# Kernel optimization log

Measured on AMD Instinct MI355X. Metric: run time of the kernel, lower is better.

The kernel has to match this reference:

```python
import jax, jax.numpy as jnp
import numpy as np

N_CROPS = 64
K = 128          # keypoints per crop (uniform ragged special case)
D = 128          # descriptor dim
KNN = 20
NQ = 20
MIN_V, MAX_V = 0.0, 1.0


def setup_inputs() -> dict:
    key = jax.random.key(0)
    k1, k2 = jax.random.split(key)
    b = N_CROPS * K
    anc = jax.random.normal(k1, (b, D), dtype=jnp.float32)
    pos = jax.random.normal(k2, (b, D), dtype=jnp.float32)
    # L2-normalized descriptors so similarities fall in the quantizer range
    anc = anc / jnp.linalg.norm(anc, axis=1, keepdims=True)
    pos = pos / jnp.linalg.norm(pos, axis=1, keepdims=True)
    kpts_crop_ids = np.full((N_CROPS,), K, dtype=np.int32)
    return {"anc_feat": anc, "pos_feat": pos, "kpts_crop_ids": kpts_crop_ids}


def _neg_cols(n_crops, k, b):
    # Static per-crop column indices into sim_neg_all (width b-1), excluding
    # the same-crop negative block [i*k, i*k + (k-1)) exactly as the torch code.
    all_c = np.arange(b - 1)
    cols = []
    for i in range(n_crops):
        c = i * k
        cols.append(np.concatenate([all_c[:c], all_c[c + k - 1:]]))
    return np.stack(cols)  # [n_crops, b-k]


def compute_ap(x, label, nq=NQ, min_v=MIN_V, max_v=MAX_V):
    # R2D2 APLoss.compute_AP: fixed 1x1-conv quantizer -> triangular bins
    a = (nq - 1) / (max_v - min_v)
    w1 = np.full(nq, -a, np.float32)
    b1 = (a * min_v + np.arange(nq, 0, -1)).astype(np.float32)
    w2 = np.full(nq, a, np.float32)
    b2 = (np.arange(2 - nq, 2) - a * min_v).astype(np.float32)
    w1[0], b1[0] = 0.0, 1.0     # first line of 1st half: horizontal
    w2[-1], b2[-1] = 0.0, 1.0   # last line of 2nd half: horizontal
    xq = x[:, None, :]
    q = jnp.minimum(w1[None, :, None] * xq + b1[None, :, None],
                    w2[None, :, None] * xq + b2[None, :, None])
    q = jnp.clip(q, 0.0)                                 # N x Q x M
    nbs = q.sum(-1)                                      # N x Q
    rec = (q * label[:, None, :]).sum(-1)                # N x Q
    prec = jnp.cumsum(rec, -1) / (1e-16 + jnp.cumsum(nbs, -1))
    rec = rec / rec.sum(-1, keepdims=True)
    return (prec * rec).sum(-1)                          # per-query AP, [N]


def reference(anc_feat, pos_feat, kpts_crop_ids):
    ks = np.asarray(kpts_crop_ids)
    assert np.all(ks == ks[0]) and int(ks[0]) > 1, "uniform crops, >1 kpt each"
    k = int(ks[0]); n_crops = ks.shape[0]; b = n_crops * k
    sim = anc_feat @ pos_feat.T                          # [b, b]
    sim_pos = jnp.diagonal(sim)[:, None]                 # [b, 1]
    # drop diagonal -> [b, b-1] (row-major off-diagonal, same as mtx[~eye])
    sim_neg_all = sim.reshape(-1)[:-1].reshape(b - 1, b + 1)[:, 1:].reshape(b, b - 1)
    cols = jnp.asarray(_neg_cols(n_crops, k, b))         # [n_crops, b-k]
    blocks = sim_neg_all.reshape(n_crops, k, b - 1)
    # exclude same-crop negatives per crop (static gather), then hard-neg top-k
    excl = jnp.take_along_axis(blocks, cols[:, None, :], axis=2)  # [n_crops, k, b-k]
    top, _ = jax.lax.top_k(excl, KNN)                    # sorted descending == sort[:, :knn]
    sim_neg = top.reshape(b, KNN)
    sim_final = jnp.concatenate([sim_pos, sim_neg], axis=1)      # [b, knn+1]
    lbl_final = jnp.zeros_like(sim_final).at[:, 0].set(1.0)
    ap = compute_ap(sim_final, lbl_final)
    return (1.0 - ap).mean(), ap.mean()
```

## Files before the change

kernel.cpp:

```cpp
#include <hip/hip_runtime.h>

#define B_TOT 8192
#define DIM 128
#define KNN 20
#define NQ 20

typedef float f32x4 __attribute__((ext_vector_type(4)));
typedef short short8 __attribute__((ext_vector_type(8)));

__device__ __forceinline__ unsigned short f2bf(float f) {
  unsigned u = __float_as_uint(f);
  return (unsigned short)((u + 0x7FFFu + ((u >> 16) & 1u)) >> 16);
}

__global__ __launch_bounds__(256) void cvt_bf16(
    const float* __restrict__ a, const float* __restrict__ p,
    unsigned short* __restrict__ ab, unsigned short* __restrict__ pb) {
  const int i = (blockIdx.x * 256 + threadIdx.x) * 4;
  const float4 va = *reinterpret_cast<const float4*>(a + i);
  const float4 vp = *reinterpret_cast<const float4*>(p + i);
  ushort4 ra, rp;
  ra.x = f2bf(va.x); ra.y = f2bf(va.y); ra.z = f2bf(va.z); ra.w = f2bf(va.w);
  rp.x = f2bf(vp.x); rp.y = f2bf(vp.y); rp.z = f2bf(vp.z); rp.w = f2bf(vp.w);
  *reinterpret_cast<ushort4*>(ab + i) = ra;
  *reinterpret_cast<ushort4*>(pb + i) = rp;
}

#define RPB 32
#define NTHR 512
#define NSTEP 64
#define CPS 128
#define SPAD 36

__global__ __launch_bounds__(512) void apk_mfma(
    const unsigned short* __restrict__ ancb,
    const unsigned short* __restrict__ posb,
    float* __restrict__ apsum)
{
  __shared__ __align__(16) float sSimT[CPS][SPAD];
  __shared__ float sTop[RPB][16][KNN];
  __shared__ float sDiag[RPB];
  __shared__ float sAp[RPB];

  const int tid = threadIdx.x;
  const int wave = tid >> 6;
  const int lane = tid & 63;
  const int rt = wave >> 2;
  const int cg = wave & 3;
  const int l15 = lane & 15;
  const int g = lane >> 4;
  const int rBase = blockIdx.x * RPB;
  const int cropLo = rBase & ~127;
  const int s_ex = cropLo >> 7;

  const int scanRow = tid & 31;
  const int scanChunk = tid >> 5;

  short8 afr[4];
  {
    const short8* arow = reinterpret_cast<const short8*>(
        ancb + (size_t)(rBase + rt * 16 + l15) * DIM);
    afr[0] = arow[0 + g];
    afr[1] = arow[4 + g];
    afr[2] = arow[8 + g];
    afr[3] = arow[12 + g];
  }

  float tk[KNN];
#pragma unroll
  for (int q = 0; q < KNN; ++q) tk[q] = -1e30f;

  const unsigned short* bbase = posb + (size_t)(cg * 32 + l15) * DIM + g * 8;

  short8 b0[2][4], b1[2][4];

#define LOADB(BUF, S)                                                         \
  {                                                                           \
    const unsigned short* bp = bbase + (size_t)(S) * (CPS * DIM);             \
    _Pragma("unroll") for (int n = 0; n < 2; ++n) {                           \
      _Pragma("unroll") for (int kk = 0; kk < 4; ++kk) {                      \
        (BUF)[n][kk] =                                                        \
            *reinterpret_cast<const short8*>(bp + n * (16 * DIM) + kk * 32);  \
      }                                                                       \
    }                                                                         \
  }

#define STEP_BODY(CUR, NXT, S)                                                \
  {                                                                           \
    if ((S) + 1 < NSTEP) LOADB(NXT, (S) + 1);                                 \
    f32x4 acc[2];                                                             \
    _Pragma("unroll") for (int n = 0; n < 2; ++n) {                           \
      acc[n] = 0.f;                                                           \
      _Pragma("unroll") for (int kk = 0; kk < 4; ++kk)                        \
        acc[n] = __builtin_amdgcn_mfma_f32_16x16x32_bf16(                     \
            afr[kk], (CUR)[n][kk], acc[n], 0, 0, 0);                          \
    }                                                                         \
    __syncthreads();                       \
    _Pragma("unroll") for (int n = 0; n < 2; ++n) {                           \
      const int c = cg * 32 + n * 16 + l15;                                   \
      *reinterpret_cast<f32x4*>(&sSimT[c][rt * 16 + g * 4]) = acc[n];         \
    }                                                                         \
    if ((S) == s_ex) {           \
      _Pragma("unroll") for (int n = 0; n < 2; ++n) {                         \
        if (cg * 32 + n * 16 == rBase - cropLo + rt * 16) {                   \
          _Pragma("unroll") for (int q = 0; q < 4; ++q)                       \
            if (l15 == 4 * g + q) sDiag[rt * 16 + l15] = acc[n][q];           \
        }                                                                     \
      }                                                                       \
    }                                                                         \
    __syncthreads();                                      \
    if ((S) != s_ex) {                                                        \
      _Pragma("unroll") for (int i = 0; i < 8; ++i) {                         \
        const float v = sSimT[scanChunk * 8 + i][scanRow];                    \
        if (v > tk[0]) {                                                      \
          float x = v;                                                        \
          _Pragma("unroll") for (int p = 0; p < KNN - 1; ++p) {               \
            const float nxt = tk[p + 1];                                      \
            tk[p] = fminf(x, nxt);                                            \
            x = fmaxf(x, nxt);                                                \
          }                                                                   \
          tk[KNN - 1] = x;                                                    \
        }                                                                     \
      }                                                                       \
    }                                                                         \
  }

  LOADB(b0, 0);
  for (int s = 0; s < NSTEP; s += 2) {
    STEP_BODY(b0, b1, s);
    STEP_BODY(b1, b0, s + 1);
  }

  __syncthreads();
  const int myRow = scanRow;
  const int myLane = scanChunk;
#pragma unroll
  for (int q = 0; q < KNN; ++q) sTop[myRow][myLane][q] = tk[q];
  __syncthreads();
  for (int step = 8; step > 0; step >>= 1) {
    if (myLane < step) {
      float out[KNN];
      int a = KNN - 1, b = KNN - 1;
#pragma unroll
      for (int o = KNN - 1; o >= 0; --o) {
        const float va = (a >= 0) ? sTop[myRow][myLane][a] : -3e30f;
        const float vb = (b >= 0) ? sTop[myRow][myLane + step][b] : -3e30f;
        if (va >= vb) { out[o] = va; --a; } else { out[o] = vb; --b; }
      }
#pragma unroll
      for (int q = 0; q < KNN; ++q) sTop[myRow][myLane][q] = out[q];
    }
    __syncthreads();
  }

  if (tid < RPB) {
    float x[KNN + 1];
    x[0] = sDiag[tid];
#pragma unroll
    for (int q = 0; q < KNN; ++q) x[q + 1] = sTop[tid][0][q];
    float cum_rec = 0.f, cum_nbs = 0.f, ap_num = 0.f;
#pragma unroll 1
    for (int qi = 0; qi < NQ; ++qi) {
      const float w1 = (qi == 0) ? 0.f : -19.f;
      const float c1 = (qi == 0) ? 1.f : (float)(20 - qi);
      const float w2 = (qi == NQ - 1) ? 0.f : 19.f;
      const float c2 = (qi == NQ - 1) ? 1.f : (float)(qi - 18);
      float nbs = 0.f, rec = 0.f;
#pragma unroll
      for (int jx = 0; jx < KNN + 1; ++jx) {
        const float xv = x[jx];
        float qv = fminf(fmaf(w1, xv, c1), fmaf(w2, xv, c2));
        qv = fmaxf(qv, 0.f);
        nbs += qv;
        if (jx == 0) rec = qv;
      }
      cum_rec += rec;
      cum_nbs += nbs;
      ap_num = fmaf(cum_rec / (1e-16f + cum_nbs), rec, ap_num);
    }
    sAp[tid] = ap_num / cum_rec;
  }
  __syncthreads();
  if (tid == 0) {
    float s = 0.f;
#pragma unroll
    for (int r = 0; r < RPB; ++r) s += sAp[r];
    atomicAdd(apsum, s);
  }
}

#define F_TM 16
#define F_TN 256
#define F_NTILE (B_TOT / F_TN)
#define F_TPR (F_TN / F_TM)
#define F_SSTRIDE 264
#define KCROP 128

__global__ __launch_bounds__(256) void apk_topk_f32(
    const float* __restrict__ anc, const float* __restrict__ pos,
    float* __restrict__ apsum)
{
  __shared__ __align__(16) float sAnc[F_TM][DIM];
  __shared__ float sSim[F_TM * F_SSTRIDE];
  __shared__ float sTop[F_TM][F_TPR][KNN];
  __shared__ float sDiag[F_TM];
  __shared__ float sAp[F_TM];

  const int tid = threadIdx.x;
  const int rowBase = blockIdx.x * F_TM;
  for (int idx = tid; idx < F_TM * DIM; idx += 256)
    sAnc[idx / DIM][idx % DIM] = anc[rowBase * DIM + idx];
  __syncthreads();

  float tk[KNN];
#pragma unroll
  for (int q = 0; q < KNN; ++q) tk[q] = -1e30f;
  const int cropLo = (rowBase >> 7) << 7;
  const int myRow = tid / F_TPR;
  const int myLane = tid % F_TPR;

  for (int t = 0; t < F_NTILE; ++t) {
    const int j = t * F_TN + tid;
    float acc[F_TM];
#pragma unroll
    for (int r = 0; r < F_TM; ++r) acc[r] = 0.f;
    const float4* pj = reinterpret_cast<const float4*>(pos + (size_t)j * DIM);
#pragma unroll 2
    for (int k4 = 0; k4 < DIM / 4; ++k4) {
      const float4 p = pj[k4];
#pragma unroll
      for (int r = 0; r < F_TM; ++r) {
        const float4 a = *reinterpret_cast<const float4*>(&sAnc[r][k4 * 4]);
        acc[r] = fmaf(p.x, a.x, acc[r]);
        acc[r] = fmaf(p.y, a.y, acc[r]);
        acc[r] = fmaf(p.z, a.z, acc[r]);
        acc[r] = fmaf(p.w, a.w, acc[r]);
      }
    }
    if (j >= rowBase && j < rowBase + F_TM) sDiag[j - rowBase] = acc[j - rowBase];
    __syncthreads();
#pragma unroll
    for (int r = 0; r < F_TM; ++r) sSim[r * F_SSTRIDE + tid] = acc[r];
    __syncthreads();
    const int jbase = t * F_TN;
#pragma unroll
    for (int q = 0; q < F_TN / F_TPR; ++q) {
      const int jj = q * F_TPR + myLane;
      const int jg = jbase + jj;
      const float v = sSim[myRow * F_SSTRIDE + jj];
      if ((unsigned)(jg - cropLo) >= (unsigned)KCROP && v > tk[0]) {
        float x = v;
#pragma unroll
        for (int p = 0; p < KNN - 1; ++p) {
          const float nxt = tk[p + 1];
          tk[p] = fminf(x, nxt);
          x = fmaxf(x, nxt);
        }
        tk[KNN - 1] = x;
      }
    }
  }
  __syncthreads();
#pragma unroll
  for (int q = 0; q < KNN; ++q) sTop[myRow][myLane][q] = tk[q];
  __syncthreads();
  for (int step = F_TPR / 2; step > 0; step >>= 1) {
    if (myLane < step) {
      float out[KNN];
      int a = KNN - 1, b = KNN - 1;
#pragma unroll
      for (int o = KNN - 1; o >= 0; --o) {
        const float va = (a >= 0) ? sTop[myRow][myLane][a] : -3e30f;
        const float vb = (b >= 0) ? sTop[myRow][myLane + step][b] : -3e30f;
        if (va >= vb) { out[o] = va; --a; } else { out[o] = vb; --b; }
      }
#pragma unroll
      for (int q = 0; q < KNN; ++q) sTop[myRow][myLane][q] = out[q];
    }
    __syncthreads();
  }
  if (tid < F_TM) {
    float x[KNN + 1];
    x[0] = sDiag[tid];
#pragma unroll
    for (int q = 0; q < KNN; ++q) x[q + 1] = sTop[tid][0][q];
    float cum_rec = 0.f, cum_nbs = 0.f, ap_num = 0.f;
#pragma unroll 1
    for (int qi = 0; qi < NQ; ++qi) {
      const float w1 = (qi == 0) ? 0.f : -19.f;
      const float c1 = (qi == 0) ? 1.f : (float)(20 - qi);
      const float w2 = (qi == NQ - 1) ? 0.f : 19.f;
      const float c2 = (qi == NQ - 1) ? 1.f : (float)(qi - 18);
      float nbs = 0.f, rec = 0.f;
#pragma unroll
      for (int jx = 0; jx < KNN + 1; ++jx) {
        const float xv = x[jx];
        float qv = fminf(fmaf(w1, xv, c1), fmaf(w2, xv, c2));
        qv = fmaxf(qv, 0.f);
        nbs += qv;
        if (jx == 0) rec = qv;
      }
      cum_rec += rec;
      cum_nbs += nbs;
      ap_num = fmaf(cum_rec / (1e-16f + cum_nbs), rec, ap_num);
    }
    sAp[tid] = ap_num / cum_rec;
  }
  __syncthreads();
  if (tid == 0) {
    float s = 0.f;
#pragma unroll
    for (int r = 0; r < F_TM; ++r) s += sAp[r];
    atomicAdd(apsum, s);
  }
}

__global__ void apk_final(const float* __restrict__ apsum, float* __restrict__ out) {
  const float m = *apsum * (1.f / (float)B_TOT);
  out[0] = 1.f - m;
  out[1] = m;
}

extern "C" void kernel_launch(void* const* d_in, const int* in_sizes, int n_in,
                              void* d_out, int out_size, void* d_ws, size_t ws_size,
                              hipStream_t stream) {
  const float* anc = (const float*)d_in[0];
  const float* pos = (const float*)d_in[1];
  const size_t bf_bytes = (size_t)B_TOT * DIM * sizeof(unsigned short);
  const size_t need = 2 * bf_bytes + 16;
  if (ws_size >= need) {
    unsigned short* ancb = (unsigned short*)d_ws;
    unsigned short* posb = ancb + (size_t)B_TOT * DIM;
    float* apsum = (float*)((char*)d_ws + 2 * bf_bytes);
    hipMemsetAsync(apsum, 0, sizeof(float), stream);
    cvt_bf16<<<(B_TOT * DIM) / (256 * 4), 256, 0, stream>>>(anc, pos, ancb, posb);
    apk_mfma<<<B_TOT / RPB, NTHR, 0, stream>>>(ancb, posb, apsum);
    apk_final<<<1, 1, 0, stream>>>(apsum, (float*)d_out);
  } else {
    float* apsum = (float*)d_ws;
    hipMemsetAsync(apsum, 0, sizeof(float), stream);
    apk_topk_f32<<<B_TOT / F_TM, 256, 0, stream>>>(anc, pos, apsum);
    apk_final<<<1, 1, 0, stream>>>(apsum, (float*)d_out);
  }
}
```

Baseline: 257.1 us.

## Split columns into slices with threshold-filtered candidate buffers and a separate reduce kernel

Replaces the per-block full-row scan with a grid of 128-row by 1024-column slices. Each wave filters MFMA results against a per-row running threshold and appends survivors to a bf16 shared buffer. The buffer is compacted to a top-20 only when it fills or at the end, and a second kernel merges the eight per-slice top lists in global memory and computes AP. This removes the per-step shared-memory transpose and the insertion sort over every similarity, in exchange for atomics, an extra kernel, and bf16-rounded candidate values that may change the result.

```diff
diff --git a/kernel.cpp b/kernel.cpp
--- a/kernel.cpp
+++ b/kernel.cpp
@@ -5,12 +5,22 @@
 #define KNN 20
 #define NQ 20
 
+#define RPB 128
+#define SLICE 1024
+#define NSLICE 8
+#define NSTEP 16
+#define CBUF 128
+#define FLAG_AT 63
+
 typedef float f32x4 __attribute__((ext_vector_type(4)));
 typedef short short8 __attribute__((ext_vector_type(8)));
 
 __device__ __forceinline__ unsigned short f2bf(float f) {
   unsigned u = __float_as_uint(f);
   return (unsigned short)((u + 0x7FFFu + ((u >> 16) & 1u)) >> 16);
+}
+__device__ __forceinline__ float bf2f(unsigned short u) {
+  return __uint_as_float(((unsigned)u) << 16);
 }
 
 __global__ __launch_bounds__(256) void cvt_bf16(
@@ -26,118 +36,308 @@
   *reinterpret_cast<ushort4*>(pb + i) = rp;
 }
 
-#define RPB 32
-#define NTHR 512
-#define NSTEP 64
-#define CPS 128
-#define SPAD 36
-
-__global__ __launch_bounds__(512) void apk_mfma(
+__global__ __launch_bounds__(512, 4) void apk_slice(
     const unsigned short* __restrict__ ancb,
     const unsigned short* __restrict__ posb,
-    float* __restrict__ apsum)
+    unsigned short* __restrict__ gTop,
+    float* __restrict__ gDiag)
 {
-  __shared__ __align__(16) float sSimT[CPS][SPAD];
-  __shared__ float sTop[RPB][16][KNN];
-  __shared__ float sDiag[RPB];
-  __shared__ float sAp[RPB];
+  __shared__ unsigned short sBuf[RPB][CBUF];
+  __shared__ float sMrg[RPB][4][KNN + 1];
+  __shared__ int sCnt[RPB];
+  __shared__ float sThr[RPB];
+  __shared__ int sFlag;
 
   const int tid = threadIdx.x;
   const int wave = tid >> 6;
   const int lane = tid & 63;
-  const int rt = wave >> 2;
-  const int cg = wave & 3;
+  const int rt = wave >> 1;
+  const int cg = wave & 1;
   const int l15 = lane & 15;
   const int g = lane >> 4;
-  const int rBase = blockIdx.x * RPB;
-  const int cropLo = rBase & ~127;
-  const int s_ex = cropLo >> 7;
-
-  const int scanRow = tid & 31;
-  const int scanChunk = tid >> 5;
-
-  short8 afr[4];
-  {
+  const int rg = blockIdx.x >> 3;
+  const int cs = blockIdx.x & 7;
+  const int rBase = rg * RPB;
+  const int sx0 = (cs == (rg >> 3)) ? (rg & 7) * 2 : -9;
+
+  for (int i = tid; i < RPB; i += 512) { sCnt[i] = 0; sThr[i] = -1e30f; }
+  if (tid == 0) sFlag = 0;
+  __syncthreads();
+
+  short8 afr[2][4];
+#pragma unroll
+  for (int rsub = 0; rsub < 2; ++rsub) {
     const short8* arow = reinterpret_cast<const short8*>(
-        ancb + (size_t)(rBase + rt * 16 + l15) * DIM);
-    afr[0] = arow[0 + g];
-    afr[1] = arow[4 + g];
-    afr[2] = arow[8 + g];
-    afr[3] = arow[12 + g];
-  }
-
+        ancb + (size_t)(rBase + rt * 32 + rsub * 16 + l15) * DIM);
+#pragma unroll
+    for (int kk = 0; kk < 4; ++kk) afr[rsub][kk] = arow[kk * 4 + g];
+  }
+
+  float thrv[2][4];
+#pragma unroll
+  for (int rsub = 0; rsub < 2; ++rsub)
+#pragma unroll
+    for (int q = 0; q < 4; ++q) thrv[rsub][q] = -1e30f;
+
+  for (int s = 0; s < NSTEP; ++s) {
+    const int c0 = cs * SLICE + s * 64 + cg * 32 + l15;
+    short8 bfr[2][4];
+#pragma unroll
+    for (int csub = 0; csub < 2; ++csub) {
+      const unsigned short* bp = posb + (size_t)(c0 + csub * 16) * DIM + g * 8;
+#pragma unroll
+      for (int kk = 0; kk < 4; ++kk)
+        bfr[csub][kk] = *reinterpret_cast<const short8*>(bp + kk * 32);
+    }
+    f32x4 acc[2][2];
+#pragma unroll
+    for (int rsub = 0; rsub < 2; ++rsub)
+#pragma unroll
+      for (int csub = 0; csub < 2; ++csub) {
+        acc[rsub][csub] = 0.f;
+#pragma unroll
+        for (int kk = 0; kk < 4; ++kk)
+          acc[rsub][csub] = __builtin_amdgcn_mfma_f32_16x16x32_bf16(
+              afr[rsub][kk], bfr[csub][kk], acc[rsub][csub], 0, 0, 0);
+      }
+
+    if (s == sx0 || s == sx0 + 1) {
+      const int soff = s - sx0;
+#pragma unroll
+      for (int rsub = 0; rsub < 2; ++rsub)
+#pragma unroll
+        for (int csub = 0; csub < 2; ++csub)
+#pragma unroll
+          for (int q = 0; q < 4; ++q) {
+            const int row_l = rt * 32 + rsub * 16 + g * 4 + q;
+            const int col_l = cg * 32 + csub * 16 + l15;
+            if (row_l == soff * 64 + col_l)
+              gDiag[rBase + row_l] = acc[rsub][csub][q];
+          }
+    } else {
+#pragma unroll
+      for (int rsub = 0; rsub < 2; ++rsub)
+#pragma unroll
+        for (int q = 0; q < 4; ++q) {
+          const int row_l = rt * 32 + rsub * 16 + g * 4 + q;
+          const float thr = thrv[rsub][q];
+          const float v0 = acc[rsub][0][q];
+          const float v1 = acc[rsub][1][q];
+          if (fmaxf(v0, v1) > thr) {
+            if (v0 > thr) {
+              const int idx = atomicAdd(&sCnt[row_l], 1);
+              if (idx >= FLAG_AT) sFlag = 1;
+              if (idx < CBUF) sBuf[row_l][idx] = f2bf(v0);
+            }
+            if (v1 > thr) {
+              const int idx = atomicAdd(&sCnt[row_l], 1);
+              if (idx >= FLAG_AT) sFlag = 1;
+              if (idx < CBUF) sBuf[row_l][idx] = f2bf(v1);
+            }
+          }
+        }
+    }
+
+    __syncthreads();
+    const int flag = sFlag;
+    __syncthreads();
+
+    if (flag != 0 || s == NSTEP - 1) {
+      const int row = tid >> 2;
+      const int h = tid & 3;
+      const int cnt = min(sCnt[row], CBUF);
+      float tk[KNN];
+#pragma unroll
+      for (int q = 0; q < KNN; ++q) tk[q] = -1e30f;
+      for (int i = 0; i < CBUF / 4; ++i) {
+        const int idx = h + i * 4;
+        if (idx < cnt) {
+          const float v = bf2f(sBuf[row][idx]);
+          if (v > tk[0]) {
+            float x = v;
+#pragma unroll
+            for (int p = 0; p < KNN - 1; ++p) {
+              const float nxt = tk[p + 1];
+              tk[p] = fminf(x, nxt);
+              x = fmaxf(x, nxt);
+            }
+            tk[KNN - 1] = x;
+          }
+        }
+      }
+#pragma unroll
+      for (int q = 0; q < KNN; ++q) sMrg[row][h][q] = tk[q];
+      if (h < 2) {
+        float out[KNN];
+        int a = KNN - 1, b = KNN - 1;
+#pragma unroll
+        for (int o = KNN - 1; o >= 0; --o) {
+          const float va = (a >= 0) ? sMrg[row][h][a] : -3e30f;
+          const float vb = (b >= 0) ? sMrg[row][h + 2][b] : -3e30f;
+          if (va >= vb) { out[o] = va; --a; } else { out[o] = vb; --b; }
+        }
+#pragma unroll
+        for (int q = 0; q < KNN; ++q) sMrg[row][h][q] = out[q];
+      }
+      if (h == 0) {
+        float out[KNN];
+        int a = KNN - 1, b = KNN - 1;
+#pragma unroll
+        for (int o = KNN - 1; o >= 0; --o) {
+          const float va = (a >= 0) ? sMrg[row][0][a] : -3e30f;
+          const float vb = (b >= 0) ? sMrg[row][1][b] : -3e30f;
+          if (va >= vb) { out[o] = va; --a; } else { out[o] = vb; --b; }
+        }
+        if (cnt > KNN) {
+          sThr[row] = out[0];
+#pragma unroll
+          for (int q = 0; q < KNN; ++q) sBuf[row][q] = f2bf(out[q]);
+          sCnt[row] = KNN;
+        }
+      }
+      if (tid == 0) sFlag = 0;
+      __syncthreads();
+#pragma unroll
+      for (int rsub = 0; rsub < 2; ++rsub)
+#pragma unroll
+        for (int q = 0; q < 4; ++q)
+          thrv[rsub][q] = sThr[rt * 32 + rsub * 16 + g * 4 + q];
+    }
+  }
+
+  for (int i = tid; i < RPB * KNN; i += 512) {
+    const int row = i / KNN, j = i % KNN;
+    const unsigned short v =
+        (j < sCnt[row]) ? sBuf[row][j] : f2bf(-1e30f);
+    gTop[(size_t)(rBase + row) * (NSLICE * KNN) + cs * KNN + j] = v;
+  }
+}
+
+__global__ __launch_bounds__(256) void apk_reduce(
+    const unsigned short* __restrict__ gTop, const float* __restrict__ gDiag,
+    float* __restrict__ apsum)
+{
+  const int row = blockIdx.x * 256 + threadIdx.x;
   float tk[KNN];
 #pragma unroll
   for (int q = 0; q < KNN; ++q) tk[q] = -1e30f;
-
-  const unsigned short* bbase = posb + (size_t)(cg * 32 + l15) * DIM + g * 8;
-
-  short8 b0[2][4], b1[2][4];
-
-#define LOADB(BUF, S)                                                         \
-  {                                                                           \
-    const unsigned short* bp = bbase + (size_t)(S) * (CPS * DIM);             \
-    _Pragma("unroll") for (int n = 0; n < 2; ++n) {                           \
-      _Pragma("unroll") for (int kk = 0; kk < 4; ++kk) {                      \
-        (BUF)[n][kk] =                                                        \
-            *reinterpret_cast<const short8*>(bp + n * (16 * DIM) + kk * 32);  \
-      }                                                                       \
-    }                                                                         \
-  }
-
-#define STEP_BODY(CUR, NXT, S)                                                \
-  {                                                                           \
-    if ((S) + 1 < NSTEP) LOADB(NXT, (S) + 1);                                 \
-    f32x4 acc[2];                                                             \
-    _Pragma("unroll") for (int n = 0; n < 2; ++n) {                           \
-      acc[n] = 0.f;                                                           \
-      _Pragma("unroll") for (int kk = 0; kk < 4; ++kk)                        \
-        acc[n] = __builtin_amdgcn_mfma_f32_16x16x32_bf16(                     \
-            afr[kk], (CUR)[n][kk], acc[n], 0, 0, 0);                          \
-    }                                                                         \
-    __syncthreads();                       \
-    _Pragma("unroll") for (int n = 0; n < 2; ++n) {                           \
-      const int c = cg * 32 + n * 16 + l15;                                   \
-      *reinterpret_cast<f32x4*>(&sSimT[c][rt * 16 + g * 4]) = acc[n];         \
-    }                                                                         \
-    if ((S) == s_ex) {           \
-      _Pragma("unroll") for (int n = 0; n < 2; ++n) {                         \
-        if (cg * 32 + n * 16 == rBase - cropLo + rt * 16) {                   \
-          _Pragma("unroll") for (int q = 0; q < 4; ++q)                       \
-            if (l15 == 4 * g + q) sDiag[rt * 16 + l15] = acc[n][q];           \
-        }                                                                     \
-      }                                                                       \
-    }                                                                         \
-    __syncthreads();                                      \
-    if ((S) != s_ex) {                                                        \
-      _Pragma("unroll") for (int i = 0; i < 8; ++i) {                         \
-        const float v = sSimT[scanChunk * 8 + i][scanRow];                    \
-        if (v > tk[0]) {                                                      \
-          float x = v;                                                        \
-          _Pragma("unroll") for (int p = 0; p < KNN - 1; ++p) {               \
-            const float nxt = tk[p + 1];                                      \
-            tk[p] = fminf(x, nxt);                                            \
-            x = fmaxf(x, nxt);                                                \
-          }                                                                   \
-          tk[KNN - 1] = x;                                                    \
-        }                                                                     \
-      }                                                                       \
-    }                                                                         \
-  }
-
-  LOADB(b0, 0);
-  for (int s = 0; s < NSTEP; s += 2) {
-    STEP_BODY(b0, b1, s);
-    STEP_BODY(b1, b0, s + 1);
-  }
-
+  const unsigned short* tp = gTop + (size_t)row * (NSLICE * KNN);
+  for (int i = 0; i < NSLICE * KNN; ++i) {
+    const float v = bf2f(tp[i]);
+    if (v > tk[0]) {
+      float x = v;
+#pragma unroll
+      for (int p = 0; p < KNN - 1; ++p) {
+        const float nxt = tk[p + 1];
+        tk[p] = fminf(x, nxt);
+        x = fmaxf(x, nxt);
+      }
+      tk[KNN - 1] = x;
+    }
+  }
+  float x[KNN + 1];
+  x[0] = gDiag[row];
+#pragma unroll
+  for (int q = 0; q < KNN; ++q) x[q + 1] = tk[q];
+  float cum_rec = 0.f, cum_nbs = 0.f, ap_num = 0.f;
+#pragma unroll 1
+  for (int qi = 0; qi < NQ; ++qi) {
+    const float w1 = (qi == 0) ? 0.f : -19.f;
+    const float c1 = (qi == 0) ? 1.f : (float)(20 - qi);
+    const float w2 = (qi == NQ - 1) ? 0.f : 19.f;
+    const float c2 = (qi == NQ - 1) ? 1.f : (float)(qi - 18);
+    float nbs = 0.f, rec = 0.f;
+#pragma unroll
+    for (int jx = 0; jx < KNN + 1; ++jx) {
+      const float xv = x[jx];
+      float qv = fminf(fmaf(w1, xv, c1), fmaf(w2, xv, c2));
+      qv = fmaxf(qv, 0.f);
+      nbs += qv;
+      if (jx == 0) rec = qv;
+    }
+    cum_rec += rec;
+    cum_nbs += nbs;
+    ap_num = fmaf(cum_rec / (1e-16f + cum_nbs), rec, ap_num);
+  }
+  float ap = ap_num / cum_rec;
+#pragma unroll
+  for (int o = 1; o < 64; o <<= 1) ap += __shfl_xor(ap, o, 64);
+  if ((threadIdx.x & 63) == 0) atomicAdd(apsum, ap);
+}
+
+#define F_TM 16
+#define F_TN 256
+#define F_NTILE (B_TOT / F_TN)
+#define F_TPR (F_TN / F_TM)
+#define F_SSTRIDE 264
+#define KCROP 128
+
+__global__ __launch_bounds__(256) void apk_topk_f32(
+    const float* __restrict__ anc, const float* __restrict__ pos,
+    float* __restrict__ apsum)
+{
+  __shared__ __align__(16) float sAnc[F_TM][DIM];
+  __shared__ float sSim[F_TM * F_SSTRIDE];
+  __shared__ float sTop[F_TM][F_TPR][KNN];
+  __shared__ float sDiag[F_TM];
+  __shared__ float sAp[F_TM];
+  const int tid = threadIdx.x;
+  const int rowBase = blockIdx.x * F_TM;
+  for (int idx = tid; idx < F_TM * DIM; idx += 256)
+    sAnc[idx / DIM][idx % DIM] = anc[rowBase * DIM + idx];
   __syncthreads();
-  const int myRow = scanRow;
-  const int myLane = scanChunk;
+  float tk[KNN];
+#pragma unroll
+  for (int q = 0; q < KNN; ++q) tk[q] = -1e30f;
+  const int cropLo = (rowBase >> 7) << 7;
+  const int myRow = tid / F_TPR;
+  const int myLane = tid % F_TPR;
+  for (int t = 0; t < F_NTILE; ++t) {
+    const int j = t * F_TN + tid;
+    float acc[F_TM];
+#pragma unroll
+    for (int r = 0; r < F_TM; ++r) acc[r] = 0.f;
+    const float4* pj = reinterpret_cast<const float4*>(pos + (size_t)j * DIM);
+#pragma unroll 2
+    for (int k4 = 0; k4 < DIM / 4; ++k4) {
+      const float4 p = pj[k4];
+#pragma unroll
+      for (int r = 0; r < F_TM; ++r) {
+        const float4 a = *reinterpret_cast<const float4*>(&sAnc[r][k4 * 4]);
+        acc[r] = fmaf(p.x, a.x, acc[r]);
+        acc[r] = fmaf(p.y, a.y, acc[r]);
+        acc[r] = fmaf(p.z, a.z, acc[r]);
+        acc[r] = fmaf(p.w, a.w, acc[r]);
+      }
+    }
+    if (j >= rowBase && j < rowBase + F_TM) sDiag[j - rowBase] = acc[j - rowBase];
+    __syncthreads();
+#pragma unroll
+    for (int r = 0; r < F_TM; ++r) sSim[r * F_SSTRIDE + tid] = acc[r];
+    __syncthreads();
+    const int jbase = t * F_TN;
+#pragma unroll
+    for (int q = 0; q < F_TN / F_TPR; ++q) {
+      const int jj = q * F_TPR + myLane;
+      const int jg = jbase + jj;
+      const float v = sSim[myRow * F_SSTRIDE + jj];
+      if ((unsigned)(jg - cropLo) >= (unsigned)KCROP && v > tk[0]) {
+        float x = v;
+#pragma unroll
+        for (int p = 0; p < KNN - 1; ++p) {
+          const float nxt = tk[p + 1];
+          tk[p] = fminf(x, nxt);
+          x = fmaxf(x, nxt);
+        }
+        tk[KNN - 1] = x;
+      }
+    }
+  }
+  __syncthreads();
 #pragma unroll
   for (int q = 0; q < KNN; ++q) sTop[myRow][myLane][q] = tk[q];
   __syncthreads();
-  for (int step = 8; step > 0; step >>= 1) {
+  for (int step = F_TPR / 2; step > 0; step >>= 1) {
     if (myLane < step) {
       float out[KNN];
       int a = KNN - 1, b = KNN - 1;
@@ -152,8 +352,7 @@
     }
     __syncthreads();
   }
-
-  if (tid < RPB) {
+  if (tid < F_TM) {
     float x[KNN + 1];
     x[0] = sDiag[tid];
 #pragma unroll
@@ -184,132 +383,6 @@
   if (tid == 0) {
     float s = 0.f;
 #pragma unroll
-    for (int r = 0; r < RPB; ++r) s += sAp[r];
-    atomicAdd(apsum, s);
-  }
-}
-
-#define F_TM 16
-#define F_TN 256
-#define F_NTILE (B_TOT / F_TN)
-#define F_TPR (F_TN / F_TM)
-#define F_SSTRIDE 264
-#define KCROP 128
-
-__global__ __launch_bounds__(256) void apk_topk_f32(
-    const float* __restrict__ anc, const float* __restrict__ pos,
-    float* __restrict__ apsum)
-{
-  __shared__ __align__(16) float sAnc[F_TM][DIM];
-  __shared__ float sSim[F_TM * F_SSTRIDE];
-  __shared__ float sTop[F_TM][F_TPR][KNN];
-  __shared__ float sDiag[F_TM];
-  __shared__ float sAp[F_TM];
-
-  const int tid = threadIdx.x;
-  const int rowBase = blockIdx.x * F_TM;
-  for (int idx = tid; idx < F_TM * DIM; idx += 256)
-    sAnc[idx / DIM][idx % DIM] = anc[rowBase * DIM + idx];
-  __syncthreads();
-
-  float tk[KNN];
-#pragma unroll
-  for (int q = 0; q < KNN; ++q) tk[q] = -1e30f;
-  const int cropLo = (rowBase >> 7) << 7;
-  const int myRow = tid / F_TPR;
-  const int myLane = tid % F_TPR;
-
-  for (int t = 0; t < F_NTILE; ++t) {
-    const int j = t * F_TN + tid;
-    float acc[F_TM];
-#pragma unroll
-    for (int r = 0; r < F_TM; ++r) acc[r] = 0.f;
-    const float4* pj = reinterpret_cast<const float4*>(pos + (size_t)j * DIM);
-#pragma unroll 2
-    for (int k4 = 0; k4 < DIM / 4; ++k4) {
-      const float4 p = pj[k4];
-#pragma unroll
-      for (int r = 0; r < F_TM; ++r) {
-        const float4 a = *reinterpret_cast<const float4*>(&sAnc[r][k4 * 4]);
-        acc[r] = fmaf(p.x, a.x, acc[r]);
-        acc[r] = fmaf(p.y, a.y, acc[r]);
-        acc[r] = fmaf(p.z, a.z, acc[r]);
-        acc[r] = fmaf(p.w, a.w, acc[r]);
-      }
-    }
-    if (j >= rowBase && j < rowBase + F_TM) sDiag[j - rowBase] = acc[j - rowBase];
-    __syncthreads();
-#pragma unroll
-    for (int r = 0; r < F_TM; ++r) sSim[r * F_SSTRIDE + tid] = acc[r];
-    __syncthreads();
-    const int jbase = t * F_TN;
-#pragma unroll
-    for (int q = 0; q < F_TN / F_TPR; ++q) {
-      const int jj = q * F_TPR + myLane;
-      const int jg = jbase + jj;
-      const float v = sSim[myRow * F_SSTRIDE + jj];
-      if ((unsigned)(jg - cropLo) >= (unsigned)KCROP && v > tk[0]) {
-        float x = v;
-#pragma unroll
-        for (int p = 0; p < KNN - 1; ++p) {
-          const float nxt = tk[p + 1];
-          tk[p] = fminf(x, nxt);
-          x = fmaxf(x, nxt);
-        }
-        tk[KNN - 1] = x;
-      }
-    }
-  }
-  __syncthreads();
-#pragma unroll
-  for (int q = 0; q < KNN; ++q) sTop[myRow][myLane][q] = tk[q];
-  __syncthreads();
-  for (int step = F_TPR / 2; step > 0; step >>= 1) {
-    if (myLane < step) {
-      float out[KNN];
-      int a = KNN - 1, b = KNN - 1;
-#pragma unroll
-      for (int o = KNN - 1; o >= 0; --o) {
-        const float va = (a >= 0) ? sTop[myRow][myLane][a] : -3e30f;
-        const float vb = (b >= 0) ? sTop[myRow][myLane + step][b] : -3e30f;
-        if (va >= vb) { out[o] = va; --a; } else { out[o] = vb; --b; }
-      }
-#pragma unroll
-      for (int q = 0; q < KNN; ++q) sTop[myRow][myLane][q] = out[q];
-    }
-    __syncthreads();
-  }
-  if (tid < F_TM) {
-    float x[KNN + 1];
-    x[0] = sDiag[tid];
-#pragma unroll
-    for (int q = 0; q < KNN; ++q) x[q + 1] = sTop[tid][0][q];
-    float cum_rec = 0.f, cum_nbs = 0.f, ap_num = 0.f;
-#pragma unroll 1
-    for (int qi = 0; qi < NQ; ++qi) {
-      const float w1 = (qi == 0) ? 0.f : -19.f;
-      const float c1 = (qi == 0) ? 1.f : (float)(20 - qi);
-      const float w2 = (qi == NQ - 1) ? 0.f : 19.f;
-      const float c2 = (qi == NQ - 1) ? 1.f : (float)(qi - 18);
-      float nbs = 0.f, rec = 0.f;
-#pragma unroll
-      for (int jx = 0; jx < KNN + 1; ++jx) {
-        const float xv = x[jx];
-        float qv = fminf(fmaf(w1, xv, c1), fmaf(w2, xv, c2));
-        qv = fmaxf(qv, 0.f);
-        nbs += qv;
-        if (jx == 0) rec = qv;
-      }
-      cum_rec += rec;
-      cum_nbs += nbs;
-      ap_num = fmaf(cum_rec / (1e-16f + cum_nbs), rec, ap_num);
-    }
-    sAp[tid] = ap_num / cum_rec;
-  }
-  __syncthreads();
-  if (tid == 0) {
-    float s = 0.f;
-#pragma unroll
     for (int r = 0; r < F_TM; ++r) s += sAp[r];
     atomicAdd(apsum, s);
   }
@@ -327,14 +400,22 @@
   const float* anc = (const float*)d_in[0];
   const float* pos = (const float*)d_in[1];
   const size_t bf_bytes = (size_t)B_TOT * DIM * sizeof(unsigned short);
-  const size_t need = 2 * bf_bytes + 16;
+  const size_t top_bytes = (size_t)B_TOT * NSLICE * KNN * sizeof(unsigned short);
+  const size_t diag_bytes = (size_t)B_TOT * sizeof(float);
+  const size_t off_top = 2 * bf_bytes;
+  const size_t off_diag = off_top + ((top_bytes + 15) & ~(size_t)15);
+  const size_t off_sum = off_diag + ((diag_bytes + 15) & ~(size_t)15);
+  const size_t need = off_sum + 16;
   if (ws_size >= need) {
     unsigned short* ancb = (unsigned short*)d_ws;
     unsigned short* posb = ancb + (size_t)B_TOT * DIM;
-    float* apsum = (float*)((char*)d_ws + 2 * bf_bytes);
+    unsigned short* gTop = (unsigned short*)((char*)d_ws + off_top);
+    float* gDiag = (float*)((char*)d_ws + off_diag);
+    float* apsum = (float*)((char*)d_ws + off_sum);
     hipMemsetAsync(apsum, 0, sizeof(float), stream);
     cvt_bf16<<<(B_TOT * DIM) / (256 * 4), 256, 0, stream>>>(anc, pos, ancb, posb);
-    apk_mfma<<<B_TOT / RPB, NTHR, 0, stream>>>(ancb, posb, apsum);
+    apk_slice<<<64 * NSLICE, 512, 0, stream>>>(ancb, posb, gTop, gDiag);
+    apk_reduce<<<B_TOT / 256, 256, 0, stream>>>(gTop, gDiag, apsum);
     apk_final<<<1, 1, 0, stream>>>(apsum, (float*)d_out);
   } else {
     float* apsum = (float*)d_ws;
```

New measurement: 247.5 us. 3.8% less time.
